# Optimization experiments

Hardware: AMD Instinct MI355X
Metric: run time of the kernel (lower is better)

Reference implementation:

```python
import jax, jax.numpy as jnp
import numpy as np

N_NODES = 20000
N_EDGES = 320000
D_IN = 256
DIMS = [512, 256, 128]
NEG_SLOPE = 0.2


def gatv2(x, src, dst, Wl, Wr, att, b, n):
    # GATv2Conv (heads=1, no self loops, no edge_attr)
    xl = x @ Wl                      # [N, D] source transform (lin_l)
    xr = x @ Wr                      # [N, D] target transform (lin_r)
    e = jax.nn.leaky_relu(xl[src] + xr[dst], NEG_SLOPE) @ att  # [E]
    # segment softmax over destination nodes
    m = jax.ops.segment_max(e, dst, num_segments=n)
    ex = jnp.exp(e - m[dst])
    s = jax.ops.segment_sum(ex, dst, num_segments=n)
    alpha = ex / (s[dst] + 1e-16)
    out = jax.ops.segment_sum(alpha[:, None] * xl[src], dst, num_segments=n)
    return out + b


def setup_inputs() -> dict:
    key = jax.random.key(0)
    ks = jax.random.split(key, 32)
    x = jax.random.normal(ks[0], (N_NODES, D_IN), dtype=jnp.float32)
    edge_index = jax.random.randint(ks[1], (2, N_EDGES), 0, N_NODES, dtype=jnp.int32)
    inp = {"x": x, "edge_index": edge_index}
    d_in = D_IN
    ki = 2
    for li, d_out in enumerate(DIMS, start=1):
        sc = 1.0 / np.sqrt(d_in)
        inp[f"Wl{li}"] = jax.random.normal(ks[ki + 0], (d_in, d_out), dtype=jnp.float32) * sc
        inp[f"Wr{li}"] = jax.random.normal(ks[ki + 1], (d_in, d_out), dtype=jnp.float32) * sc
        inp[f"att{li}"] = jax.random.normal(ks[ki + 2], (d_out,), dtype=jnp.float32) * (1.0 / np.sqrt(d_out))
        inp[f"bc{li}"] = jnp.zeros((d_out,), dtype=jnp.float32)
        inp[f"Ws{li}"] = jax.random.normal(ks[ki + 3], (d_in, d_out), dtype=jnp.float32) * sc
        inp[f"bs{li}"] = jnp.zeros((d_out,), dtype=jnp.float32)
        ki += 4
        d_in = d_out
    return inp


def reference(x, edge_index,
              Wl1, Wr1, att1, bc1, Ws1, bs1,
              Wl2, Wr2, att2, bc2, Ws2, bs2,
              Wl3, Wr3, att3, bc3, Ws3, bs3):
    src, dst = edge_index[0], edge_index[1]
    n = x.shape[0]
    h = gatv2(x, src, dst, Wl1, Wr1, att1, bc1, n) + (x @ Ws1 + bs1)
    h = jax.nn.relu(h)
    h = gatv2(h, src, dst, Wl2, Wr2, att2, bc2, n) + (h @ Ws2 + bs2)
    h = jax.nn.relu(h)
    h = gatv2(h, src, dst, Wl3, Wr3, att3, bc3, n) + (h @ Ws3 + bs3)
    return h
```

## Files before the change

### kernel.cpp

```cpp
#include <hip/hip_runtime.h>
#include <hip/hip_bf16.h>
#include <math.h>

#define N_NODES 20000
#define N_EDGES 320000
#define MAXDEG 64

typedef _Float16 f16x8 __attribute__((ext_vector_type(8)));
typedef _Float16 h2 __attribute__((ext_vector_type(2)));
typedef float f32x4 __attribute__((ext_vector_type(4)));

__device__ __forceinline__ unsigned short f2h_bits(float f) {
    _Float16 h = (_Float16)f;
    return __builtin_bit_cast(unsigned short, h);
}

typedef const unsigned int __attribute__((address_space(1)))* gas_ptr;
typedef unsigned int __attribute__((address_space(3)))* las_ptr;
__device__ __forceinline__ void gld16(const unsigned short* g, unsigned short* l) {
    __builtin_amdgcn_global_load_lds((gas_ptr)(const void*)g, (las_ptr)(void*)l, 16, 0, 0);
}

__global__ void scatter_kernel(const int* __restrict__ src, const int* __restrict__ dst,
                               int* __restrict__ cnt, int* __restrict__ csr_pad, int E) {
    int i = blockIdx.x * blockDim.x + threadIdx.x;
    if (i < E) {
        int d = dst[i];
        int pos = atomicAdd(&cnt[d], 1);
        if (pos < MAXDEG) csr_pad[(d << 6) + pos] = src[i];
    }
}

struct PrepJobs {
    const float* W[9];
    unsigned short* Wt[9];
    int K[9];
    int D[9];
    int tbeg[10];
    const float* x;
    unsigned short* xh;
    int nconv4;
    int nconvb;
    int* cnt;
};
__global__ __launch_bounds__(256) void prep_kernel(PrepJobs jb) {
    int bid = blockIdx.x;
    int ntile = jb.tbeg[9];
    if (bid < ntile) {
        __shared__ float ld[32][33];
        int job = 0;
        while (bid >= jb.tbeg[job + 1]) ++job;
        int tl = bid - jb.tbeg[job];
        int K = jb.K[job], D = jb.D[job];
        int TK = K >> 5;
        int td = tl / TK, tk = tl - td * TK;
        int k0 = tk << 5, d0 = td << 5;
        int t = threadIdx.x;
        int c = t & 31, r0 = (t >> 5) << 2;
        const float* Wp = jb.W[job];
#pragma unroll
        for (int jj = 0; jj < 4; ++jj)
            ld[r0 + jj][c] = Wp[(size_t)(k0 + r0 + jj) * D + d0 + c];
        __syncthreads();
        unsigned short* Wtp = jb.Wt[job];
#pragma unroll
        for (int jj = 0; jj < 4; ++jj) {
            int dr = r0 + jj;
            Wtp[(size_t)(d0 + dr) * K + k0 + c] = f2h_bits(ld[c][dr]);
        }
    } else if (bid < ntile + jb.nconvb) {
        int cidx = (bid - ntile) * 256 + (int)threadIdx.x;
        if (cidx < jb.nconv4) {
            int base = cidx * 4;
            float4 v = *(const float4*)(jb.x + base);
            uint2 pk;
            pk.x = (unsigned int)f2h_bits(v.x) | ((unsigned int)f2h_bits(v.y) << 16);
            pk.y = (unsigned int)f2h_bits(v.z) | ((unsigned int)f2h_bits(v.w) << 16);
            *(uint2*)(jb.xh + base) = pk;
        }
    } else {
        int i = (bid - ntile - jb.nconvb) * 256 + (int)threadIdx.x;
        if (i < N_NODES) jb.cnt[i] = 0;
    }
}

template <int SEED_F32>
__global__ __launch_bounds__(256) void gemm3_kernel(
        const unsigned short* __restrict__ A,
        const unsigned short* __restrict__ Bt,
        unsigned short* __restrict__ xlh,
        unsigned short* __restrict__ xrh,
        unsigned short* __restrict__ seedh,
        float* __restrict__ seedf,
        const float* __restrict__ b1,
        const float* __restrict__ b2,
        int M, int K, int D) {
    __shared__ __align__(16) unsigned short Asl[128 * 64];
    __shared__ __align__(16) unsigned short Bsl[128 * 64];

    int NC = (3 * D) >> 7;
    int MT = (M + 127) >> 7;
    int g = blockIdx.x;
    int xcd = g & 7, slot = g >> 3;
    int m_local = slot / NC, c = slot - m_local * NC;
    int mt = m_local * 8 + xcd;
    if (mt >= MT) return;

    int tid = threadIdx.x;
    int wave = tid >> 6, lane = tid & 63;
    int q = lane >> 4, t = lane & 15;
    int wm = (wave & 1) * 64, wn = (wave >> 1) * 64;
    int bm = mt << 7;
    int bn_all = c << 7;
    int seg = bn_all / D;
    int bn = bn_all - seg * D;

    f32x4 acc[4][4];
#pragma unroll
    for (int i = 0; i < 4; ++i)
#pragma unroll
        for (int j = 0; j < 4; ++j) acc[i][j] = (f32x4){0.f, 0.f, 0.f, 0.f};

    for (int k0 = 0; k0 < K; k0 += 64) {
#pragma unroll
        for (int rnd = 0; rnd < 4; ++rnd) {
            int ch = rnd * 256 + tid;
            int row = ch >> 3, part = ch & 7;
            int sw = part ^ (row & 7);
            int gr = bm + row; if (gr >= M) gr = M - 1;
            gld16(A + (size_t)gr * K + k0 + sw * 8,
                  Asl + (rnd * 256 + wave * 64) * 8);
        }
#pragma unroll
        for (int rnd = 0; rnd < 4; ++rnd) {
            int ch = rnd * 256 + tid;
            int row = ch >> 3, part = ch & 7;
            int sw = part ^ (row & 7);
            gld16(Bt + (size_t)(bn_all + row) * K + k0 + sw * 8,
                  Bsl + (rnd * 256 + wave * 64) * 8);
        }
        __syncthreads();

#pragma unroll
        for (int kk = 0; kk < 2; ++kk) {
            f16x8 an[4], am[4];
#pragma unroll
            for (int jn = 0; jn < 4; ++jn) {
                int rb = wn + jn * 16 + t;
                an[jn] = *(const f16x8*)(Bsl + rb * 64 + ((((kk << 2) | q) ^ (rb & 7)) << 3));
            }
#pragma unroll
            for (int im = 0; im < 4; ++im) {
                int ra = wm + im * 16 + t;
                am[im] = *(const f16x8*)(Asl + ra * 64 + ((((kk << 2) | q) ^ (ra & 7)) << 3));
            }
#pragma unroll
            for (int jn = 0; jn < 4; ++jn)
#pragma unroll
                for (int im = 0; im < 4; ++im)
                    acc[jn][im] = __builtin_amdgcn_mfma_f32_16x16x32_f16(an[jn], am[im], acc[jn][im], 0, 0, 0);
        }
        __syncthreads();
    }

#pragma unroll
    for (int jn = 0; jn < 4; ++jn) {
        int n0 = bn + wn + jn * 16 + q * 4;
        float bx = 0.f, by = 0.f, bz = 0.f, bw = 0.f;
        if (seg == 2) {
            float4 bb1 = *(const float4*)(b1 + n0);
            float4 bb2 = *(const float4*)(b2 + n0);
            bx = bb1.x + bb2.x; by = bb1.y + bb2.y;
            bz = bb1.z + bb2.z; bw = bb1.w + bb2.w;
        }
#pragma unroll
        for (int im = 0; im < 4; ++im) {
            int m = bm + wm + im * 16 + t;
            if (m < M) {
                float v0 = acc[jn][im][0] + bx;
                float v1 = acc[jn][im][1] + by;
                float v2 = acc[jn][im][2] + bz;
                float v3 = acc[jn][im][3] + bw;
                size_t idx = (size_t)m * D + n0;
                if (seg == 2 && SEED_F32) {
                    *(float4*)(seedf + idx) = make_float4(v0, v1, v2, v3);
                } else {
                    uint2 pk;
                    pk.x = (unsigned int)f2h_bits(v0) | ((unsigned int)f2h_bits(v1) << 16);
                    pk.y = (unsigned int)f2h_bits(v2) | ((unsigned int)f2h_bits(v3) << 16);
                    unsigned short* dstp = (seg == 0) ? xlh : (seg == 1) ? xrh : seedh;
                    *(uint2*)(dstp + idx) = pk;
                }
            }
        }
    }
}

template <int D, int SEED_H, int WRITE_H, int RELU>
__global__ __launch_bounds__(128) void fused_agg_kernel(
        const unsigned short* __restrict__ xl,
        const unsigned short* __restrict__ xr,
        const float* __restrict__ att,
        const int* __restrict__ cnt,
        const int* __restrict__ csr_pad,
        const unsigned short* __restrict__ seedh,
        const float* __restrict__ seedf,
        float* __restrict__ outf,
        unsigned short* __restrict__ outh) {
    constexpr int VPL = D / 64;
    constexpr int HP = VPL / 2;
    typedef _Float16 hvec __attribute__((ext_vector_type(VPL)));

    int wave = threadIdx.x >> 6, lane = threadIdx.x & 63;
    int n = blockIdx.x * 2 + wave;
    if (n >= N_NODES) return;
    int cn = cnt[n]; if (cn > MAXDEG) cn = MAXDEG;
    int beg = n << 6;
    int end = beg + cn;

    h2 xr_h[HP], att_h[HP];
    hvec xrv = *(const hvec*)(xr + (size_t)n * D + lane * VPL);
#pragma unroll
    for (int pp = 0; pp < HP; ++pp) {
        xr_h[pp] = (h2){xrv[2 * pp], xrv[2 * pp + 1]};
        att_h[pp] = (h2){(_Float16)att[lane * VPL + 2 * pp],
                         (_Float16)att[lane * VPL + 2 * pp + 1]};
    }

    float acc[VPL];
#pragma unroll
    for (int v = 0; v < VPL; ++v) acc[v] = 0.f;
    float m = -INFINITY, s = 0.f;

    const _Float16 c02 = (_Float16)0.2f;
    int lb0 = lane & 1;
    int lb1 = lane & 2;

    int nfull = cn >> 2;
    int j = beg;
    int i0 = 0, i1 = 0, i2 = 0, i3 = 0;
    if (nfull > 0) {
        i0 = csr_pad[beg]; i1 = csr_pad[beg + 1];
        i2 = csr_pad[beg + 2]; i3 = csr_pad[beg + 3];
    }
    for (int b = 0; b < nfull; ++b) {
        int s0 = i0, s1 = i1, s2 = i2, s3 = i3;
        int jn4 = j + 4;
        if (b + 1 < nfull) {
            i0 = csr_pad[jn4]; i1 = csr_pad[jn4 + 1];
            i2 = csr_pad[jn4 + 2]; i3 = csr_pad[jn4 + 3];
        }
        hvec x0 = *(const hvec*)(xl + (size_t)s0 * D + lane * VPL);
        hvec x1 = *(const hvec*)(xl + (size_t)s1 * D + lane * VPL);
        hvec x2 = *(const hvec*)(xl + (size_t)s2 * D + lane * VPL);
        hvec x3 = *(const hvec*)(xl + (size_t)s3 * D + lane * VPL);
        float p0 = 0.f, p1 = 0.f, p2 = 0.f, p3 = 0.f;
#pragma unroll
        for (int pp = 0; pp < HP; ++pp) {
            h2 a0 = (h2){x0[2 * pp], x0[2 * pp + 1]};
            h2 a1 = (h2){x1[2 * pp], x1[2 * pp + 1]};
            h2 a2 = (h2){x2[2 * pp], x2[2 * pp + 1]};
            h2 a3 = (h2){x3[2 * pp], x3[2 * pp + 1]};
            h2 z0 = a0 + xr_h[pp];
            h2 z1 = a1 + xr_h[pp];
            h2 z2 = a2 + xr_h[pp];
            h2 z3 = a3 + xr_h[pp];
            h2 l0 = __builtin_elementwise_max(z0, z0 * c02);
            h2 l1 = __builtin_elementwise_max(z1, z1 * c02);
            h2 l2 = __builtin_elementwise_max(z2, z2 * c02);
            h2 l3 = __builtin_elementwise_max(z3, z3 * c02);
#if __has_builtin(__builtin_amdgcn_fdot2)
            p0 = __builtin_amdgcn_fdot2(l0, att_h[pp], p0, false);
            p1 = __builtin_amdgcn_fdot2(l1, att_h[pp], p1, false);
            p2 = __builtin_amdgcn_fdot2(l2, att_h[pp], p2, false);
            p3 = __builtin_amdgcn_fdot2(l3, att_h[pp], p3, false);
#else
            p0 += (float)l0.x * (float)att_h[pp].x + (float)l0.y * (float)att_h[pp].y;
            p1 += (float)l1.x * (float)att_h[pp].x + (float)l1.y * (float)att_h[pp].y;
            p2 += (float)l2.x * (float)att_h[pp].x + (float)l2.y * (float)att_h[pp].y;
            p3 += (float)l3.x * (float)att_h[pp].x + (float)l3.y * (float)att_h[pp].y;
#endif
        }
        float k0 = lb0 ? p1 : p0, sn0 = lb0 ? p0 : p1;
        float k1 = lb0 ? p3 : p2, sn1 = lb0 ? p2 : p3;
        k0 += __shfl_xor(sn0, 1, 64);
        k1 += __shfl_xor(sn1, 1, 64);
        float k = lb1 ? k1 : k0, sn = lb1 ? k0 : k1;
        k += __shfl_xor(sn, 2, 64);
        k += __shfl_xor(k, 4, 64);
        k += __shfl_xor(k, 8, 64);
        k += __shfl_xor(k, 16, 64);
        k += __shfl_xor(k, 32, 64);
        float q0 = __shfl(k, 0, 64);
        float q1 = __shfl(k, 1, 64);
        float q2 = __shfl(k, 2, 64);
        float q3 = __shfl(k, 3, 64);

        float mn = fmaxf(m, fmaxf(fmaxf(q0, q1), fmaxf(q2, q3)));
        float sc = __expf(m - mn);
        float e0 = __expf(q0 - mn);
        float e1 = __expf(q1 - mn);
        float e2 = __expf(q2 - mn);
        float e3 = __expf(q3 - mn);
        s = s * sc + e0 + e1 + e2 + e3;
#pragma unroll
        for (int v = 0; v < VPL; ++v)
            acc[v] = acc[v] * sc + e0 * (float)x0[v] + e1 * (float)x1[v]
                                 + e2 * (float)x2[v] + e3 * (float)x3[v];
        m = mn;
        j = jn4;
    }
    for (; j < end; ++j) {
        int s0 = csr_pad[j];
        hvec x0 = *(const hvec*)(xl + (size_t)s0 * D + lane * VPL);
        float p0 = 0.f;
#pragma unroll
        for (int pp = 0; pp < HP; ++pp) {
            h2 a0 = (h2){x0[2 * pp], x0[2 * pp + 1]};
            h2 z0 = a0 + xr_h[pp];
            h2 l0 = __builtin_elementwise_max(z0, z0 * c02);
#if __has_builtin(__builtin_amdgcn_fdot2)
            p0 = __builtin_amdgcn_fdot2(l0, att_h[pp], p0, false);
#else
            p0 += (float)l0.x * (float)att_h[pp].x + (float)l0.y * (float)att_h[pp].y;
#endif
        }
#pragma unroll
        for (int o = 32; o > 0; o >>= 1) p0 += __shfl_xor(p0, o, 64);
        float mn = fmaxf(m, p0);
        float sc = __expf(m - mn);
        float e0 = __expf(p0 - mn);
        s = s * sc + e0;
#pragma unroll
        for (int v = 0; v < VPL; ++v) acc[v] = acc[v] * sc + e0 * (float)x0[v];
        m = mn;
    }

    float sinv = 1.0f / (s + 1e-16f);
    size_t base = (size_t)n * D + lane * VPL;
    float sd[VPL];
    if (SEED_H) {
        hvec sv = *(const hvec*)(seedh + base);
#pragma unroll
        for (int v = 0; v < VPL; ++v) sd[v] = (float)sv[v];
    } else {
#pragma unroll
        for (int v = 0; v < VPL; ++v) sd[v] = seedf[base + v];
    }
#pragma unroll
    for (int v = 0; v < VPL; ++v) {
        float val = sd[v] + acc[v] * sinv;
        if (RELU) val = fmaxf(val, 0.f);
        if (WRITE_H) outh[base + v] = f2h_bits(val);
        else         outf[base + v] = val;
    }
}

static void run_layer(const unsigned short* hact, int K, int D,
                      const unsigned short* Wcat,
                      const float* att, const float* bc, const float* bs,
                      unsigned short* xlh, unsigned short* xrh,
                      unsigned short* seedh, float* seedf,
                      const int* cnt, const int* csr_pad,
                      float* outf, unsigned short* outh, int final_layer,
                      hipStream_t stream) {
    int NC = 3 * D / 128;
    int MT = (N_NODES + 127) / 128;
    int nblk = 8 * ((MT + 7) / 8) * NC;
    if (final_layer)
        hipLaunchKernelGGL((gemm3_kernel<1>), dim3(nblk), dim3(256), 0, stream, hact, Wcat,
                           xlh, xrh, (unsigned short*)nullptr, seedf, bs, bc, N_NODES, K, D);
    else
        hipLaunchKernelGGL((gemm3_kernel<0>), dim3(nblk), dim3(256), 0, stream, hact, Wcat,
                           xlh, xrh, seedh, (float*)nullptr, bs, bc, N_NODES, K, D);

    dim3 agrid((N_NODES + 1) / 2);
    if (D == 512) {
        hipLaunchKernelGGL((fused_agg_kernel<512, 1, 1, 1>), agrid, dim3(128), 0, stream,
                           xlh, xrh, att, cnt, csr_pad, seedh, (const float*)nullptr,
                           (float*)nullptr, outh);
    } else if (D == 256) {
        hipLaunchKernelGGL((fused_agg_kernel<256, 1, 1, 1>), agrid, dim3(128), 0, stream,
                           xlh, xrh, att, cnt, csr_pad, seedh, (const float*)nullptr,
                           (float*)nullptr, outh);
    } else {
        hipLaunchKernelGGL((fused_agg_kernel<128, 0, 0, 0>), agrid, dim3(128), 0, stream,
                           xlh, xrh, att, cnt, csr_pad, (const unsigned short*)nullptr, seedf,
                           outf, (unsigned short*)nullptr);
    }
}

extern "C" void kernel_launch(void* const* d_in, const int* in_sizes, int n_in,
                              void* d_out, int out_size, void* d_ws, size_t ws_size,
                              hipStream_t stream) {
    const float* x = (const float*)d_in[0];
    const int* ei = (const int*)d_in[1];
    const int* src = ei;
    const int* dst = ei + N_EDGES;

    const float* Wl1 = (const float*)d_in[2];
    const float* Wr1 = (const float*)d_in[3];
    const float* att1 = (const float*)d_in[4];
    const float* bc1 = (const float*)d_in[5];
    const float* Ws1 = (const float*)d_in[6];
    const float* bs1 = (const float*)d_in[7];
    const float* Wl2 = (const float*)d_in[8];
    const float* Wr2 = (const float*)d_in[9];
    const float* att2 = (const float*)d_in[10];
    const float* bc2 = (const float*)d_in[11];
    const float* Ws2 = (const float*)d_in[12];
    const float* bs2 = (const float*)d_in[13];
    const float* Wl3 = (const float*)d_in[14];
    const float* Wr3 = (const float*)d_in[15];
    const float* att3 = (const float*)d_in[16];
    const float* bc3 = (const float*)d_in[17];
    const float* Ws3 = (const float*)d_in[18];
    const float* bs3 = (const float*)d_in[19];

    const size_t NF = (size_t)N_NODES * 512;
    const size_t NH = (size_t)N_NODES * 256;
    unsigned short* xlh   = (unsigned short*)d_ws;
    unsigned short* xrh   = xlh + NF;
    unsigned short* seedh = xrh + NF;
    unsigned short* xhf   = seedh + NF;
    unsigned short* h1h   = xhf + NH;
    unsigned short* h2h   = h1h + NF;
    unsigned short* Wcat1 = h2h + NH;
    unsigned short* Wcat2 = Wcat1 + 3 * 512 * 256;
    unsigned short* Wcat3 = Wcat2 + 3 * 256 * 512;
    int* cnt     = (int*)(Wcat3 + 3 * 128 * 256);
    int* csr_pad = cnt + N_NODES;
    size_t needed = (size_t)((char*)(csr_pad + (size_t)N_NODES * MAXDEG) - (char*)d_ws);
    if (ws_size < needed) return;

    {
        PrepJobs jb;
        const float* Ws_[9]  = {Wl1, Wr1, Ws1, Wl2, Wr2, Ws2, Wl3, Wr3, Ws3};
        unsigned short* Wt_[9] = {Wcat1, Wcat1 + 512 * 256, Wcat1 + 2 * 512 * 256,
                                  Wcat2, Wcat2 + 256 * 512, Wcat2 + 2 * 256 * 512,
                                  Wcat3, Wcat3 + 128 * 256, Wcat3 + 2 * 128 * 256};
        int K_[9] = {256, 256, 256, 512, 512, 512, 256, 256, 256};
        int D_[9] = {512, 512, 512, 256, 256, 256, 128, 128, 128};
        int o = 0;
        for (int i = 0; i < 9; ++i) {
            jb.W[i] = Ws_[i]; jb.Wt[i] = Wt_[i]; jb.K[i] = K_[i]; jb.D[i] = D_[i];
            jb.tbeg[i] = o; o += (K_[i] >> 5) * (D_[i] >> 5);
        }
        jb.tbeg[9] = o;
        jb.x = x;
        jb.xh = xhf;
        jb.nconv4 = N_NODES * 256 / 4;
        jb.nconvb = (jb.nconv4 + 255) / 256;
        jb.cnt = cnt;
        int nzerob = (N_NODES + 255) / 256;
        hipLaunchKernelGGL(prep_kernel, dim3(o + jb.nconvb + nzerob), dim3(256), 0, stream, jb);
    }
    hipLaunchKernelGGL(scatter_kernel, dim3((N_EDGES + 255) / 256), dim3(256), 0, stream,
                       src, dst, cnt, csr_pad, N_EDGES);

    run_layer(xhf, 256, 512, Wcat1, att1, bc1, bs1,
              xlh, xrh, seedh, (float*)nullptr, cnt, csr_pad,
              (float*)nullptr, h1h, 0, stream);
    run_layer(h1h, 512, 256, Wcat2, att2, bc2, bs2,
              xlh, xrh, seedh, (float*)nullptr, cnt, csr_pad,
              (float*)nullptr, h2h, 0, stream);
    run_layer(h2h, 256, 128, Wcat3, att3, bc3, bs3,
              xlh, xrh, (unsigned short*)nullptr, (float*)d_out, cnt, csr_pad,
              (float*)d_out, (unsigned short*)nullptr, 1, stream);
}
```

Measured before the change: 308.6 us.

## Double-buffer LDS tiles in GEMM to overlap global loads with MFMA

Splits the A and B shared-memory tiles into two buffers. The next K-slice is prefetched via global_load_lds while MFMAs run on the current one, using explicit vmcnt waits and raw barriers in place of __syncthreads. The goal is to hide global-to-LDS latency in the fused xl/xr/skip GEMM. This doubles LDS use to 64KB per block, which may lower occupancy, and it depends on the hand-written vmcnt counts being correct.

```diff
diff --git a/kernel.cpp b/kernel.cpp
--- a/kernel.cpp
+++ b/kernel.cpp
@@ -95,8 +95,8 @@
         const float* __restrict__ b1,
         const float* __restrict__ b2,
         int M, int K, int D) {
-    __shared__ __align__(16) unsigned short Asl[128 * 64];
-    __shared__ __align__(16) unsigned short Bsl[128 * 64];
+    __shared__ __align__(16) unsigned short Asl[2][128 * 64];
+    __shared__ __align__(16) unsigned short Bsl[2][128 * 64];
 
     int NC = (3 * D) >> 7;
     int MT = (M + 127) >> 7;
@@ -121,25 +121,56 @@
 #pragma unroll
         for (int j = 0; j < 4; ++j) acc[i][j] = (f32x4){0.f, 0.f, 0.f, 0.f};
 
-    for (int k0 = 0; k0 < K; k0 += 64) {
+    int niter = K >> 6;
+
+    {
 #pragma unroll
         for (int rnd = 0; rnd < 4; ++rnd) {
             int ch = rnd * 256 + tid;
             int row = ch >> 3, part = ch & 7;
             int sw = part ^ (row & 7);
             int gr = bm + row; if (gr >= M) gr = M - 1;
-            gld16(A + (size_t)gr * K + k0 + sw * 8,
-                  Asl + (rnd * 256 + wave * 64) * 8);
+            gld16(A + (size_t)gr * K + sw * 8,
+                  &Asl[0][(rnd * 256 + wave * 64) * 8]);
         }
 #pragma unroll
         for (int rnd = 0; rnd < 4; ++rnd) {
             int ch = rnd * 256 + tid;
             int row = ch >> 3, part = ch & 7;
             int sw = part ^ (row & 7);
-            gld16(Bt + (size_t)(bn_all + row) * K + k0 + sw * 8,
-                  Bsl + (rnd * 256 + wave * 64) * 8);
-        }
-        __syncthreads();
+            gld16(Bt + (size_t)(bn_all + row) * K + sw * 8,
+                  &Bsl[0][(rnd * 256 + wave * 64) * 8]);
+        }
+    }
+
+    for (int i = 0; i < niter; ++i) {
+        int cur = i & 1;
+        if (i + 1 < niter) {
+            int k0 = (i + 1) << 6;
+            int nb = cur ^ 1;
+#pragma unroll
+            for (int rnd = 0; rnd < 4; ++rnd) {
+                int ch = rnd * 256 + tid;
+                int row = ch >> 3, part = ch & 7;
+                int sw = part ^ (row & 7);
+                int gr = bm + row; if (gr >= M) gr = M - 1;
+                gld16(A + (size_t)gr * K + k0 + sw * 8,
+                      &Asl[nb][(rnd * 256 + wave * 64) * 8]);
+            }
+#pragma unroll
+            for (int rnd = 0; rnd < 4; ++rnd) {
+                int ch = rnd * 256 + tid;
+                int row = ch >> 3, part = ch & 7;
+                int sw = part ^ (row & 7);
+                gld16(Bt + (size_t)(bn_all + row) * K + k0 + sw * 8,
+                      &Bsl[nb][(rnd * 256 + wave * 64) * 8]);
+            }
+            asm volatile("s_waitcnt vmcnt(8)" ::: "memory");
+        } else {
+            asm volatile("s_waitcnt vmcnt(0)" ::: "memory");
+        }
+        __builtin_amdgcn_s_barrier();
+        __builtin_amdgcn_sched_barrier(0);
 
 #pragma unroll
         for (int kk = 0; kk < 2; ++kk) {
@@ -147,12 +178,12 @@
 #pragma unroll
             for (int jn = 0; jn < 4; ++jn) {
                 int rb = wn + jn * 16 + t;
-                an[jn] = *(const f16x8*)(Bsl + rb * 64 + ((((kk << 2) | q) ^ (rb & 7)) << 3));
+                an[jn] = *(const f16x8*)(&Bsl[cur][rb * 64 + ((((kk << 2) | q) ^ (rb & 7)) << 3)]);
             }
 #pragma unroll
             for (int im = 0; im < 4; ++im) {
                 int ra = wm + im * 16 + t;
-                am[im] = *(const f16x8*)(Asl + ra * 64 + ((((kk << 2) | q) ^ (ra & 7)) << 3));
+                am[im] = *(const f16x8*)(&Asl[cur][ra * 64 + ((((kk << 2) | q) ^ (ra & 7)) << 3)]);
             }
 #pragma unroll
             for (int jn = 0; jn < 4; ++jn)
@@ -160,7 +191,8 @@
                 for (int im = 0; im < 4; ++im)
                     acc[jn][im] = __builtin_amdgcn_mfma_f32_16x16x32_f16(an[jn], am[im], acc[jn][im], 0, 0, 0);
         }
-        __syncthreads();
+        __builtin_amdgcn_s_barrier();
+        __builtin_amdgcn_sched_barrier(0);
     }
 
 #pragma unroll
```

Result: no change. 304.8 us, median of 2 (-1.2%).
